# Performance work log

Hardware: AMD Instinct MI355X
Metric: run time of the kernel (lower is better)

Reference implementation:

```python
import jax, jax.numpy as jnp
import numpy as np

B = 2048          # batch of tree nodes
C = 256           # num_classes (GRU input size)
HS = 512          # h_size
H2 = 2 * HS       # GRU hidden size
D = 8             # max_output_degree


def setup_inputs() -> dict:
    key = jax.random.key(0)
    ks = jax.random.split(key, 12)
    s_ih = 1.0 / np.sqrt(C)
    s_h = 1.0 / np.sqrt(H2)
    return {
        "parent_output_label": jax.random.uniform(ks[0], (B, C), dtype=jnp.float32),
        "parent_h": jax.random.normal(ks[1], (B, HS), dtype=jnp.float32),
        "encoding": jax.random.normal(ks[2], (B, HS), dtype=jnp.float32),
        # stacked GRUCell params over the D output-degree slots
        "W_ih": jax.random.uniform(ks[3], (D, 3 * H2, C), jnp.float32, -s_ih, s_ih),
        "W_hh": jax.random.uniform(ks[4], (D, 3 * H2, H2), jnp.float32, -s_h, s_h),
        "b_ih": jax.random.uniform(ks[5], (D, 3 * H2), jnp.float32, -s_h, s_h),
        "b_hh": jax.random.uniform(ks[6], (D, 3 * H2), jnp.float32, -s_h, s_h),
        # stacked linear_probs (2h -> 1) and linear_hiddens (2h -> h)
        "W_p": jax.random.uniform(ks[7], (D, H2), jnp.float32, -s_h, s_h),
        "b_p": jax.random.uniform(ks[8], (D,), jnp.float32, -s_h, s_h),
        "W_h": jax.random.uniform(ks[9], (D, HS, H2), jnp.float32, -s_h, s_h),
        "b_h": jax.random.uniform(ks[10], (D, HS), jnp.float32, -s_h, s_h),
    }


def _compute_state_probs(x, h0, W_ih, W_hh, b_ih, b_hh, W_p, b_p, W_h, b_h):
    # x: [B, C], h0: [B, H2]. All D GRUCells fused into batched einsums.
    gi = jnp.einsum("bc,dgc->bdg", x, W_ih) + b_ih[None]        # [B, D, 3*H2]
    gh = jnp.einsum("bh,dgh->bdg", h0, W_hh) + b_hh[None]       # [B, D, 3*H2]
    i_r, i_z, i_n = jnp.split(gi, 3, axis=-1)
    h_r, h_z, h_n = jnp.split(gh, 3, axis=-1)
    r = jax.nn.sigmoid(i_r + h_r)
    z = jax.nn.sigmoid(i_z + h_z)
    n = jnp.tanh(i_n + r * h_n)
    hn = (1.0 - z) * n + z * h0[:, None, :]                      # [B, D, H2]
    probs = jax.nn.sigmoid(jnp.einsum("bdh,dh->bd", hn, W_p) + b_p[None])  # [B, D]
    hc = jnp.einsum("bdh,dkh->bdk", hn, W_h) + b_h[None]         # [B, D, HS]
    h = jnp.tanh(jnp.sum(hc, axis=1))                            # activ over summed slot hiddens
    return h, probs


def reference(parent_output_label, parent_h, encoding,
              W_ih, W_hh, b_ih, b_hh, W_p, b_p, W_h, b_h):
    h0 = jnp.concatenate([parent_h, encoding], axis=1)           # [B, 2*h_size]
    return _compute_state_probs(parent_output_label, h0,
                                W_ih, W_hh, b_ih, b_hh, W_p, b_p, W_h, b_h)
```

## Files before the change

### kernel.cpp

```cpp
#include <hip/hip_runtime.h>


#define B_   2048
#define C_   256
#define HS_  512
#define H2_  1024
#define G3_  3072
#define D_   8
#define NG_  24576
#define KF_  1280

typedef __attribute__((ext_vector_type(8))) short bfrag;
typedef __attribute__((ext_vector_type(4))) float f32x4;
typedef __attribute__((ext_vector_type(4))) unsigned short u16x4;
typedef __attribute__((ext_vector_type(2))) unsigned int u32x2;

static __device__ __forceinline__ unsigned short f2bf(float f) {
  unsigned u = __float_as_uint(f);
  u = (u + 0x7FFFu + ((u >> 16) & 1u)) >> 16;
  return (unsigned short)u;
}
static __device__ __forceinline__ float bf2f(unsigned short s) {
  return __uint_as_float(((unsigned)s) << 16);
}
static __device__ __forceinline__ unsigned pack2bf(float a, float b) {
  return ((unsigned)f2bf(b) << 16) | (unsigned)f2bf(a);
}
static __device__ __forceinline__ float fast_sigmoid(float x) {
  return 1.f / (1.f + __expf(-x));
}
static __device__ __forceinline__ float fast_tanh(float x) {
  return 1.f - 2.f / (__expf(2.f * x) + 1.f);
}

__device__ __forceinline__ void load16(const void* g, void* l) {
  __builtin_amdgcn_global_load_lds((const __attribute__((address_space(1))) void*)g,
                                   (__attribute__((address_space(3))) void*)l,
                                   16, 0, 0);
}

__global__ __launch_bounds__(256) void pack_kernel(
    const float* __restrict__ x, const float* __restrict__ ph,
    const float* __restrict__ enc, const float* __restrict__ Wih,
    const float* __restrict__ Whh, const float* __restrict__ Wh,
    unsigned short* __restrict__ A, unsigned short* __restrict__ Bf,
    unsigned short* __restrict__ BWh)
{
  const long long total4 = 38273024LL / 4;
  const long long stride = (long long)gridDim.x * blockDim.x;
  for (long long i = (long long)blockIdx.x * blockDim.x + threadIdx.x;
       i < total4; i += stride) {
    long long o = i * 4;
    const float* src;
    unsigned short* dst;
    if (o < 2621440) {
      unsigned rel = (unsigned)o;
      unsigned b = rel / 1280u, c = rel % 1280u;
      if (c < 256) src = x + (size_t)b * 256 + c;
      else if (c < 768) src = ph + (size_t)b * 512 + (c - 256);
      else src = enc + (size_t)b * 512 + (c - 768);
      dst = A + rel;
    } else if (o < 34078720) {
      unsigned rel = (unsigned)(o - 2621440);
      unsigned grow = rel / 1280u, c = rel % 1280u;
      unsigned d = grow / 3072u, rr = grow - d * 3072u;
      unsigned hbb = rr / 192u, r3 = rr - hbb * 192u;
      unsigned g = r3 >> 6, hl = r3 & 63u;
      unsigned srow = d * 3072u + g * 1024u + hbb * 64u + hl;
      src = (c < 256) ? (Wih + (size_t)srow * 256 + c)
                      : (Whh + (size_t)srow * 1024 + (c - 256));
      dst = Bf + rel;
    } else {
      unsigned rel = (unsigned)(o - 34078720);
      unsigned kk = rel >> 13;
      unsigned r2 = rel & 8191;
      unsigned d = r2 >> 10, hh = r2 & 1023;
      src = Wh + ((size_t)d * 524288 + (size_t)kk * 1024 + hh);
      dst = BWh + rel;
    }
    float4 v = *(const float4*)src;
    ushort4 w;
    w.x = f2bf(v.x); w.y = f2bf(v.y); w.z = f2bf(v.z); w.w = f2bf(v.w);
    *(ushort4*)dst = w;
  }
}

__global__ __launch_bounds__(512, 2) void mega_gemm(
    const unsigned short* __restrict__ A, const unsigned short* __restrict__ Bf,
    const float* __restrict__ ph, const float* __restrict__ enc,
    const float* __restrict__ bih, const float* __restrict__ bhh,
    const float* __restrict__ Wp, unsigned short* __restrict__ hn,
    float* __restrict__ pacc)
{
  extern __shared__ char lds[];
  const int t = threadIdx.x;
  const int wave = t >> 6, lane = t & 63;
  const int wr = wave >> 2, wc = wave & 3;
  const int la = lane & 15, ls = lane >> 4;

  const int orig = blockIdx.x;
  const int xcd = orig & 7;
  const int l = orig >> 3;
  const int brow8 = (xcd & 1) * 4 + (l & 3);
  const int cb = ((l >> 2) << 2) + (xcd >> 1);
  const int brow = brow8 << 8;
  const int bcol = cb * 192;
  const int d = cb >> 4, hb = cb & 15;
  const int nT = 20;

  const int srr = t >> 3;
  const int ssc = ((t & 7) ^ ((t >> 3) & 7)) << 3;

  auto stageA = [&](int kt, int buf, int hf) {
    const unsigned short* src = A + (size_t)(brow + hf * 128 + srr) * KF_ + kt * 64 + ssc;
    char* dst = lds + buf * 32768 + hf * 16384 + t * 16;
    load16(src, dst);
    load16(src + (size_t)64 * KF_, dst + 8192);
  };
  auto stageB = [&](int kt, int buf, int th) {
    const unsigned short* src = Bf + (size_t)(bcol + th * 64 + srr) * KF_ + kt * 64 + ssc;
    char* dst = lds + 65536 + buf * 24576 + th * 8192 + t * 16;
    load16(src, dst);
  };

  stageA(0, 0, 0); stageA(0, 0, 1);
  stageB(0, 0, 0); stageB(0, 0, 1); stageB(0, 0, 2);
  stageA(1, 1, 0); stageA(1, 1, 1);
  stageB(1, 1, 0); stageB(1, 1, 1); stageB(1, 1, 2);
  asm volatile("s_waitcnt vmcnt(7)" ::: "memory");
  __builtin_amdgcn_s_barrier();

  f32x4 acc[8][3];
#pragma unroll
  for (int m = 0; m < 8; ++m)
#pragma unroll
    for (int n = 0; n < 3; ++n) acc[m][n] = (f32x4){0.f, 0.f, 0.f, 0.f};

  const int c0 = (ls << 4) ^ ((la & 7) << 4);

#pragma unroll 1
  for (int kt = 0; kt < nT; ++kt) {
    const int buf = kt & 1;
    const char* ab = lds + buf * 32768 + wr * 16384;
    const char* bb = lds + 65536 + buf * 24576;
    bfrag a0[8], a1[8], b0[3], b1[3];

#pragma unroll
    for (int m = 0; m < 8; ++m)
      a0[m] = *(const bfrag*)(ab + (m * 16 + la) * 128 + c0);
#pragma unroll
    for (int n = 0; n < 3; ++n) {
      const int r = wc * 48 + n * 16 + la;
      b0[n] = *(const bfrag*)(bb + (r >> 6) * 8192 + (r & 63) * 128 + c0);
    }
#pragma unroll
    for (int m = 0; m < 8; ++m)
      a1[m] = *(const bfrag*)(ab + (m * 16 + la) * 128 + (c0 ^ 64));
#pragma unroll
    for (int n = 0; n < 3; ++n) {
      const int r = wc * 48 + n * 16 + la;
      b1[n] = *(const bfrag*)(bb + (r >> 6) * 8192 + (r & 63) * 128 + (c0 ^ 64));
    }
    __builtin_amdgcn_s_barrier();
    __builtin_amdgcn_s_setprio(1);
#pragma unroll
    for (int m = 0; m < 8; ++m)
#pragma unroll
      for (int n = 0; n < 3; ++n)
        acc[m][n] = __builtin_amdgcn_mfma_f32_16x16x32_bf16(a0[m], b0[n], acc[m][n], 0, 0, 0);
    __builtin_amdgcn_s_setprio(0);
    asm volatile("s_waitcnt lgkmcnt(0)" ::: "memory");
    __builtin_amdgcn_s_barrier();

    if (kt + 2 < nT) {
      stageA(kt + 2, buf, 0);
      stageA(kt + 2, buf, 1);
      stageB(kt + 2, buf, 0);
      stageB(kt + 2, buf, 1);
      stageB(kt + 2, buf, 2);
    }
    __builtin_amdgcn_s_setprio(1);
#pragma unroll
    for (int m = 0; m < 8; ++m)
#pragma unroll
      for (int n = 0; n < 3; ++n)
        acc[m][n] = __builtin_amdgcn_mfma_f32_16x16x32_bf16(a1[m], b1[n], acc[m][n], 0, 0, 0);
    __builtin_amdgcn_s_setprio(0);
    if (kt + 2 < nT) {
      asm volatile("s_waitcnt vmcnt(7)" ::: "memory");
    } else {
      asm volatile("s_waitcnt vmcnt(0)" ::: "memory");
    }
    __builtin_amdgcn_s_barrier();

    if (kt == 3) {
#pragma unroll
      for (int m = 0; m < 8; ++m)
#pragma unroll
        for (int n = 0; n < 3; ++n) {
          const int colb = wc * 48 + n * 16;
          if (colb >= 128) {
            const int hl = (colb & 63) + la;
            const int row = wr * 128 + m * 16 + ls * 4;
            u32x2 v;
            v[0] = pack2bf(acc[m][n][0], acc[m][n][1]);
            v[1] = pack2bf(acc[m][n][2], acc[m][n][3]);
            *(u32x2*)(lds + 114688 + hl * 520 + row * 2) = v;
            acc[m][n] = (f32x4){0.f, 0.f, 0.f, 0.f};
          }
        }
    }
  }

  __syncthreads();
#pragma unroll
  for (int m = 0; m < 8; ++m)
#pragma unroll
    for (int n = 0; n < 3; ++n) {
      const int col = wc * 48 + n * 16 + la;
      const int row = wr * 128 + m * 16 + ls * 4;
      u32x2 v;
      v[0] = pack2bf(acc[m][n][0], acc[m][n][1]);
      v[1] = pack2bf(acc[m][n][2], acc[m][n][3]);
      *(u32x2*)(lds + col * 520 + row * 2) = v;
    }
  __syncthreads();

  const unsigned short* lu = (const unsigned short*)lds;
  const int row = t >> 1, half = t & 1;
  const int grow = brow + row;
  const int hbase = hb * 64 + half * 32;
  const float* h0p = (hb < 8) ? (ph + (size_t)grow * 512 + hbase)
                              : (enc + (size_t)grow * 512 + hbase - 512);
  float partial = 0.f;
  u16x4 st;
#pragma unroll
  for (int jj = 0; jj < 8; ++jj) {
    const int hg = hbase + jj * 4;
    const f32x4 br_ = *(const f32x4*)(bih + d * 3072 + hg);
    const f32x4 hr_ = *(const f32x4*)(bhh + d * 3072 + hg);
    const f32x4 bz_ = *(const f32x4*)(bih + d * 3072 + 1024 + hg);
    const f32x4 hz_ = *(const f32x4*)(bhh + d * 3072 + 1024 + hg);
    const f32x4 bn_ = *(const f32x4*)(bih + d * 3072 + 2048 + hg);
    const f32x4 hn_ = *(const f32x4*)(bhh + d * 3072 + 2048 + hg);
    const f32x4 wp_ = *(const f32x4*)(Wp + d * 1024 + hg);
    const f32x4 h0_ = *(const f32x4*)(h0p + jj * 4);
#pragma unroll
    for (int i = 0; i < 4; ++i) {
      const int hl = half * 32 + jj * 4 + i;
      const float rp = bf2f(lu[hl * 260 + row]);
      const float zp = bf2f(lu[(64 + hl) * 260 + row]);
      const float sp = bf2f(lu[(128 + hl) * 260 + row]);
      const float ip = bf2f(lu[57344 + hl * 260 + row]);
      const float r = fast_sigmoid(rp + br_[i] + hr_[i]);
      const float z = fast_sigmoid(zp + bz_[i] + hz_[i]);
      const float nn = fast_tanh(ip + bn_[i] + r * (sp + hn_[i]));
      const float hv = (1.f - z) * nn + z * h0_[i];
      st[i] = f2bf(hv);
      partial += hv * wp_[i];
    }
    *(u16x4*)(hn + (size_t)grow * 8192 + d * 1024 + hg) = st;
  }
  partial += __shfl_xor(partial, 1);
  if (!half) atomicAdd(pacc + (size_t)grow * 8 + d, partial);
}

__global__ __launch_bounds__(256) void gemm_bt(
    const unsigned short* __restrict__ A, const unsigned short* __restrict__ Bt,
    float* __restrict__ out, int M, int N, int K, int kPerSlice)
{
  __shared__ unsigned short sA[128 * 32];
  __shared__ unsigned short sB[128 * 32];
  const int t = threadIdx.x;
  const int wave = t >> 6, lane = t & 63;
  const int wr = wave >> 1, wc = wave & 1;

  const int orig = blockIdx.x;
  const int x7 = orig & 7;
  const int y = (x7 << 1) | ((orig >> 3) & 1);
  const int l2 = orig >> 4;
  const int xcol = l2 & 3;
  const int z = l2 >> 2;
  const int brow = y << 7;
  const int bcol = xcol << 7;
  const int kOff = z * kPerSlice;

  f32x4 acc[4][4];
#pragma unroll
  for (int m = 0; m < 4; m++)
#pragma unroll
    for (int n = 0; n < 4; n++) acc[m][n] = (f32x4){0.f, 0.f, 0.f, 0.f};

  const int srow = t >> 2;
  const int scol = (t & 3) << 3;
  const unsigned short* aSrc = A + (size_t)(brow + srow) * K + kOff + scol;
  const unsigned short* bSrc = Bt + (size_t)(bcol + srow) * K + kOff + scol;
  const size_t rowStep = (size_t)64 * K;
  unsigned short* dA0 = sA + wave * 512;
  unsigned short* dA1 = sA + 2048 + wave * 512;
  unsigned short* dB0 = sB + wave * 512;
  unsigned short* dB1 = sB + 2048 + wave * 512;

  const int la = lane & 15;
  const int lk = (lane >> 4) << 3;
  const int kSteps = kPerSlice >> 5;

  for (int ks = 0; ks < kSteps; ++ks) {
    load16(aSrc, dA0);
    load16(aSrc + rowStep, dA1);
    load16(bSrc, dB0);
    load16(bSrc + rowStep, dB1);
    aSrc += 32; bSrc += 32;
    __syncthreads();
    bfrag aF[4], bF[4];
#pragma unroll
    for (int m = 0; m < 4; m++)
      aF[m] = *(const bfrag*)&sA[(wr * 64 + m * 16 + la) * 32 + lk];
#pragma unroll
    for (int n = 0; n < 4; n++)
      bF[n] = *(const bfrag*)&sB[(wc * 64 + n * 16 + la) * 32 + lk];
#pragma unroll
    for (int m = 0; m < 4; m++)
#pragma unroll
      for (int n = 0; n < 4; n++)
        acc[m][n] = __builtin_amdgcn_mfma_f32_16x16x32_bf16(aF[m], bF[n], acc[m][n], 0, 0, 0);
    __syncthreads();
  }

  const int orow = brow + wr * 64 + (lane >> 4) * 4;
  const int ocol = bcol + wc * 64 + la;
  float* o = out + (size_t)z * ((size_t)M * N);
#pragma unroll
  for (int m = 0; m < 4; m++) {
    const int rb = orow + m * 16;
#pragma unroll
    for (int n = 0; n < 4; n++) {
      const int cbb = ocol + n * 16;
#pragma unroll
      for (int r = 0; r < 4; r++)
        o[(size_t)(rb + r) * N + cbb] = acc[m][n][r];
    }
  }
}

__global__ __launch_bounds__(256) void reduce_h_kernel(
    const float* __restrict__ part, const float* __restrict__ b_h,
    float* __restrict__ hout)
{
  const int idx = blockIdx.x * 256 + threadIdx.x;
  const int kk = idx & 511;
  float s = 0.f;
#pragma unroll
  for (int sl = 0; sl < 16; ++sl) s += part[(size_t)sl * 1048576 + idx];
  float bias = 0.f;
#pragma unroll
  for (int d = 0; d < 8; ++d) bias += b_h[d * 512 + kk];
  hout[idx] = fast_tanh(s + bias);
}

__global__ __launch_bounds__(256) void probs_final(
    const float* __restrict__ pacc, const float* __restrict__ b_p,
    float* __restrict__ pout)
{
  const int i = blockIdx.x * 256 + threadIdx.x;
  pout[i] = fast_sigmoid(pacc[i] + b_p[i & 7]);
}

extern "C" void kernel_launch(void* const* d_in, const int* in_sizes, int n_in,
                              void* d_out, int out_size, void* d_ws, size_t ws_size,
                              hipStream_t stream) {
  const float* x   = (const float*)d_in[0];
  const float* ph  = (const float*)d_in[1];
  const float* enc = (const float*)d_in[2];
  const float* Wih = (const float*)d_in[3];
  const float* Whh = (const float*)d_in[4];
  const float* bih = (const float*)d_in[5];
  const float* bhh = (const float*)d_in[6];
  const float* Wp  = (const float*)d_in[7];
  const float* bp  = (const float*)d_in[8];
  const float* Wh  = (const float*)d_in[9];
  const float* bh  = (const float*)d_in[10];
  float* out = (float*)d_out;
  char* ws = (char*)d_ws;

  unsigned short* A    = (unsigned short*)(ws + 0);
  unsigned short* Bf   = (unsigned short*)(ws + 5242880);
  unsigned short* BWh  = (unsigned short*)(ws + 68157440);
  unsigned short* hn   = (unsigned short*)(ws + 76546048);
  float*          part = (float*)(ws + 110100480);
  float*          pacc = (float*)(ws + 177209344);

  hipFuncSetAttribute((const void*)mega_gemm,
                      hipFuncAttributeMaxDynamicSharedMemorySize, 147968);

  hipMemsetAsync(pacc, 0, 2048 * 8 * sizeof(float), stream);

  pack_kernel<<<2048, 256, 0, stream>>>(x, ph, enc, Wih, Whh, Wh, A, Bf, BWh);

  mega_gemm<<<1024, 512, 147968, stream>>>(A, Bf, ph, enc, bih, bhh, Wp, hn, pacc);

  gemm_bt<<<1024, 256, 0, stream>>>(hn, BWh, part, B_, HS_, 8192, 512);

  reduce_h_kernel<<<4096, 256, 0, stream>>>(part, bh, out);

  probs_final<<<64, 256, 0, stream>>>(pacc, bp, out + 1048576);
}
```

Before: 265.4 us.

## Halve mega_gemm row tile to 128 and keep input-gate partials in registers

The fused GRU GEMM now uses 128-row tiles instead of 256, doubling the grid to 2048 blocks and cutting LDS use to about 80 KB, so more blocks can be resident per CU (launch bounds raised to 4). The early input-gate partial sums are kept packed in registers and written to LDS only during the epilogue, instead of needing a dedicated LDS region for the whole main loop. The epilogue is remapped to four segments per row, with an LDS reduction in place of the shuffle before the atomic add. The trade-off is lower data reuse per block, since each weight tile is now loaded twice as often, plus extra register pressure under the tighter launch bound.

```diff
diff --git a/kernel.cpp b/kernel.cpp
--- a/kernel.cpp
+++ b/kernel.cpp
@@ -9,6 +9,10 @@
 #define D_   8
 #define NG_  24576
 #define KF_  1280
+
+#define PRE_OFF 0
+#define IN_OFF  50688
+#define RED_OFF 67584
 
 typedef __attribute__((ext_vector_type(8))) short bfrag;
 typedef __attribute__((ext_vector_type(4))) float f32x4;
@@ -85,7 +89,7 @@
   }
 }
 
-__global__ __launch_bounds__(512, 2) void mega_gemm(
+__global__ __launch_bounds__(512, 4) void mega_gemm(
     const unsigned short* __restrict__ A, const unsigned short* __restrict__ Bf,
     const float* __restrict__ ph, const float* __restrict__ enc,
     const float* __restrict__ bih, const float* __restrict__ bhh,
@@ -101,9 +105,9 @@
   const int orig = blockIdx.x;
   const int xcd = orig & 7;
   const int l = orig >> 3;
-  const int brow8 = (xcd & 1) * 4 + (l & 3);
-  const int cb = ((l >> 2) << 2) + (xcd >> 1);
-  const int brow = brow8 << 8;
+  const int brow16 = (xcd & 1) * 8 + (l & 7);
+  const int cb = ((l >> 3) << 2) + (xcd >> 1);
+  const int brow = brow16 << 7;
   const int bcol = cb * 192;
   const int d = cb >> 4, hb = cb & 15;
   const int nT = 20;
@@ -112,14 +116,13 @@
   const int ssc = ((t & 7) ^ ((t >> 3) & 7)) << 3;
 
   auto stageA = [&](int kt, int buf, int hf) {
-    const unsigned short* src = A + (size_t)(brow + hf * 128 + srr) * KF_ + kt * 64 + ssc;
-    char* dst = lds + buf * 32768 + hf * 16384 + t * 16;
+    const unsigned short* src = A + (size_t)(brow + hf * 64 + srr) * KF_ + kt * 64 + ssc;
+    char* dst = lds + buf * 16384 + hf * 8192 + t * 16;
     load16(src, dst);
-    load16(src + (size_t)64 * KF_, dst + 8192);
   };
   auto stageB = [&](int kt, int buf, int th) {
     const unsigned short* src = Bf + (size_t)(bcol + th * 64 + srr) * KF_ + kt * 64 + ssc;
-    char* dst = lds + 65536 + buf * 24576 + th * 8192 + t * 16;
+    char* dst = lds + 32768 + buf * 24576 + th * 8192 + t * 16;
     load16(src, dst);
   };
 
@@ -127,12 +130,13 @@
   stageB(0, 0, 0); stageB(0, 0, 1); stageB(0, 0, 2);
   stageA(1, 1, 0); stageA(1, 1, 1);
   stageB(1, 1, 0); stageB(1, 1, 1); stageB(1, 1, 2);
-  asm volatile("s_waitcnt vmcnt(7)" ::: "memory");
+  asm volatile("s_waitcnt vmcnt(5)" ::: "memory");
   __builtin_amdgcn_s_barrier();
 
-  f32x4 acc[8][3];
-#pragma unroll
-  for (int m = 0; m < 8; ++m)
+  f32x4 acc[4][3];
+  u32x2 in_pk[4][3];
+#pragma unroll
+  for (int m = 0; m < 4; ++m)
 #pragma unroll
     for (int n = 0; n < 3; ++n) acc[m][n] = (f32x4){0.f, 0.f, 0.f, 0.f};
 
@@ -141,21 +145,21 @@
 #pragma unroll 1
   for (int kt = 0; kt < nT; ++kt) {
     const int buf = kt & 1;
-    const char* ab = lds + buf * 32768 + wr * 16384;
-    const char* bb = lds + 65536 + buf * 24576;
-    bfrag a0[8], a1[8], b0[3], b1[3];
-
-#pragma unroll
-    for (int m = 0; m < 8; ++m)
-      a0[m] = *(const bfrag*)(ab + (m * 16 + la) * 128 + c0);
+    const char* ab = lds + buf * 16384;
+    const char* bb = lds + 32768 + buf * 24576;
+    bfrag a0[4], a1[4], b0[3], b1[3];
+
+#pragma unroll
+    for (int m = 0; m < 4; ++m)
+      a0[m] = *(const bfrag*)(ab + (wr * 64 + m * 16 + la) * 128 + c0);
 #pragma unroll
     for (int n = 0; n < 3; ++n) {
       const int r = wc * 48 + n * 16 + la;
       b0[n] = *(const bfrag*)(bb + (r >> 6) * 8192 + (r & 63) * 128 + c0);
     }
 #pragma unroll
-    for (int m = 0; m < 8; ++m)
-      a1[m] = *(const bfrag*)(ab + (m * 16 + la) * 128 + (c0 ^ 64));
+    for (int m = 0; m < 4; ++m)
+      a1[m] = *(const bfrag*)(ab + (wr * 64 + m * 16 + la) * 128 + (c0 ^ 64));
 #pragma unroll
     for (int n = 0; n < 3; ++n) {
       const int r = wc * 48 + n * 16 + la;
@@ -164,7 +168,7 @@
     __builtin_amdgcn_s_barrier();
     __builtin_amdgcn_s_setprio(1);
 #pragma unroll
-    for (int m = 0; m < 8; ++m)
+    for (int m = 0; m < 4; ++m)
 #pragma unroll
       for (int n = 0; n < 3; ++n)
         acc[m][n] = __builtin_amdgcn_mfma_f32_16x16x32_bf16(a0[m], b0[n], acc[m][n], 0, 0, 0);
@@ -181,13 +185,13 @@
     }
     __builtin_amdgcn_s_setprio(1);
 #pragma unroll
-    for (int m = 0; m < 8; ++m)
+    for (int m = 0; m < 4; ++m)
 #pragma unroll
       for (int n = 0; n < 3; ++n)
         acc[m][n] = __builtin_amdgcn_mfma_f32_16x16x32_bf16(a1[m], b1[n], acc[m][n], 0, 0, 0);
     __builtin_amdgcn_s_setprio(0);
     if (kt + 2 < nT) {
-      asm volatile("s_waitcnt vmcnt(7)" ::: "memory");
+      asm volatile("s_waitcnt vmcnt(5)" ::: "memory");
     } else {
       asm volatile("s_waitcnt vmcnt(0)" ::: "memory");
     }
@@ -195,17 +199,12 @@
 
     if (kt == 3) {
 #pragma unroll
-      for (int m = 0; m < 8; ++m)
+      for (int m = 0; m < 4; ++m)
 #pragma unroll
         for (int n = 0; n < 3; ++n) {
-          const int colb = wc * 48 + n * 16;
-          if (colb >= 128) {
-            const int hl = (colb & 63) + la;
-            const int row = wr * 128 + m * 16 + ls * 4;
-            u32x2 v;
-            v[0] = pack2bf(acc[m][n][0], acc[m][n][1]);
-            v[1] = pack2bf(acc[m][n][2], acc[m][n][3]);
-            *(u32x2*)(lds + 114688 + hl * 520 + row * 2) = v;
+          if (wc * 48 + n * 16 >= 128) {
+            in_pk[m][n][0] = pack2bf(acc[m][n][0], acc[m][n][1]);
+            in_pk[m][n][1] = pack2bf(acc[m][n][2], acc[m][n][3]);
             acc[m][n] = (f32x4){0.f, 0.f, 0.f, 0.f};
           }
         }
@@ -214,28 +213,32 @@
 
   __syncthreads();
 #pragma unroll
-  for (int m = 0; m < 8; ++m)
+  for (int m = 0; m < 4; ++m)
 #pragma unroll
     for (int n = 0; n < 3; ++n) {
       const int col = wc * 48 + n * 16 + la;
-      const int row = wr * 128 + m * 16 + ls * 4;
+      const int row = wr * 64 + m * 16 + ls * 4;
       u32x2 v;
       v[0] = pack2bf(acc[m][n][0], acc[m][n][1]);
       v[1] = pack2bf(acc[m][n][2], acc[m][n][3]);
-      *(u32x2*)(lds + col * 520 + row * 2) = v;
+      *(u32x2*)(lds + PRE_OFF + col * 264 + row * 2) = v;
+      if (wc * 48 + n * 16 >= 128)
+        *(u32x2*)(lds + IN_OFF + (col - 128) * 264 + row * 2) = in_pk[m][n];
     }
   __syncthreads();
 
-  const unsigned short* lu = (const unsigned short*)lds;
-  const int row = t >> 1, half = t & 1;
+  const unsigned short* lu = (const unsigned short*)(lds + PRE_OFF);
+  const unsigned short* li = (const unsigned short*)(lds + IN_OFF);
+  float* red = (float*)(lds + RED_OFF);
+  const int row = t & 127, seg = t >> 7;
   const int grow = brow + row;
-  const int hbase = hb * 64 + half * 32;
+  const int hbase = hb * 64 + seg * 16;
   const float* h0p = (hb < 8) ? (ph + (size_t)grow * 512 + hbase)
                               : (enc + (size_t)grow * 512 + hbase - 512);
   float partial = 0.f;
   u16x4 st;
 #pragma unroll
-  for (int jj = 0; jj < 8; ++jj) {
+  for (int jj = 0; jj < 4; ++jj) {
     const int hg = hbase + jj * 4;
     const f32x4 br_ = *(const f32x4*)(bih + d * 3072 + hg);
     const f32x4 hr_ = *(const f32x4*)(bhh + d * 3072 + hg);
@@ -247,11 +250,11 @@
     const f32x4 h0_ = *(const f32x4*)(h0p + jj * 4);
 #pragma unroll
     for (int i = 0; i < 4; ++i) {
-      const int hl = half * 32 + jj * 4 + i;
-      const float rp = bf2f(lu[hl * 260 + row]);
-      const float zp = bf2f(lu[(64 + hl) * 260 + row]);
-      const float sp = bf2f(lu[(128 + hl) * 260 + row]);
-      const float ip = bf2f(lu[57344 + hl * 260 + row]);
+      const int hl = seg * 16 + jj * 4 + i;
+      const float rp = bf2f(lu[hl * 132 + row]);
+      const float zp = bf2f(lu[(64 + hl) * 132 + row]);
+      const float sp = bf2f(lu[(128 + hl) * 132 + row]);
+      const float ip = bf2f(li[hl * 132 + row]);
       const float r = fast_sigmoid(rp + br_[i] + hr_[i]);
       const float z = fast_sigmoid(zp + bz_[i] + hz_[i]);
       const float nn = fast_tanh(ip + bn_[i] + r * (sp + hn_[i]));
@@ -261,8 +264,12 @@
     }
     *(u16x4*)(hn + (size_t)grow * 8192 + d * 1024 + hg) = st;
   }
-  partial += __shfl_xor(partial, 1);
-  if (!half) atomicAdd(pacc + (size_t)grow * 8 + d, partial);
+  red[row * 4 + seg] = partial;
+  __syncthreads();
+  if (t < 128) {
+    float s = red[t * 4] + red[t * 4 + 1] + red[t * 4 + 2] + red[t * 4 + 3];
+    atomicAdd(pacc + (size_t)(brow + t) * 8 + d, s);
+  }
 }
 
 __global__ __launch_bounds__(256) void gemm_bt(
@@ -391,13 +398,13 @@
   float*          pacc = (float*)(ws + 177209344);
 
   hipFuncSetAttribute((const void*)mega_gemm,
-                      hipFuncAttributeMaxDynamicSharedMemorySize, 147968);
+                      hipFuncAttributeMaxDynamicSharedMemorySize, 81920);
 
   hipMemsetAsync(pacc, 0, 2048 * 8 * sizeof(float), stream);
 
   pack_kernel<<<2048, 256, 0, stream>>>(x, ph, enc, Wih, Whh, Wh, A, Bf, BWh);
 
-  mega_gemm<<<1024, 512, 147968, stream>>>(A, Bf, ph, enc, bih, bhh, Wp, hn, pacc);
+  mega_gemm<<<2048, 512, 81920, stream>>>(A, Bf, ph, enc, bih, bhh, Wp, hn, pacc);
 
   gemm_bt<<<1024, 256, 0, stream>>>(hn, BWh, part, B_, HS_, 8192, 512);
 
```

After: 347.7 us. +31.0%, slower.
